# Kernel optimization log

Measured on AMD Instinct MI355X. Metric: run time of the kernel, lower is better.

## Reference

```python
import jax, jax.numpy as jnp
import numpy as np

B, S, HS = 2, 2048, 4096
NH, NKV = 32, 32
HD = HS // NH
INTER = 11008
VOCAB = 32000
EPS = 1e-6
ROPE_BASE = 10000.0


def setup_inputs() -> dict:
    key = jax.random.key(0)
    ks = jax.random.split(key, 16)
    sc = 0.02
    return {
        "hidden_states": jax.random.normal(ks[0], (B, S, HS), jnp.float32),
        "input_ids": jax.random.randint(ks[1], (B, S), 0, VOCAB, jnp.int32),
        "position_ids": jnp.arange(S, dtype=jnp.int32)[None, :],
        "embed": jax.random.normal(ks[2], (VOCAB, HS), jnp.float32) * sc,
        "fc_w": jax.random.normal(ks[3], (HS, 2 * HS), jnp.float32) * sc,
        "fc_b": jnp.zeros((HS,), jnp.float32),
        "q_w": jax.random.normal(ks[4], (NH * HD, HS), jnp.float32) * sc,
        "k_w": jax.random.normal(ks[5], (NKV * HD, HS), jnp.float32) * sc,
        "v_w": jax.random.normal(ks[6], (NKV * HD, HS), jnp.float32) * sc,
        "o_w": jax.random.normal(ks[7], (HS, NH * HD), jnp.float32) * sc,
        "gate_w": jax.random.normal(ks[8], (INTER, HS), jnp.float32) * sc,
        "up_w": jax.random.normal(ks[9], (INTER, HS), jnp.float32) * sc,
        "down_w": jax.random.normal(ks[10], (HS, INTER), jnp.float32) * sc,
        "post_ln_w": jnp.ones((HS,), jnp.float32),
    }


def _rotate_half(x):
    x1, x2 = jnp.split(x, 2, axis=-1)
    return jnp.concatenate((-x2, x1), axis=-1)


def _rms_norm(x, w, eps=EPS):
    x32 = x.astype(jnp.float32)
    x32 = x32 * jax.lax.rsqrt(jnp.mean(x32 * x32, axis=-1, keepdims=True) + eps)
    return (w * x32).astype(x.dtype)


def _forward(hidden_states, input_ids, position_ids, embed, fc_w, fc_b,
             q_w, k_w, v_w, o_w, gate_w, up_w, down_w, post_ln_w):
    # Embedding lookup (detached in original via no_grad)
    embeds = jax.lax.stop_gradient(embed[input_ids])  # [B,S,HS]
    h = jnp.concatenate((embeds, hidden_states), axis=-1) @ fc_w.T + fc_b  # [B,S,HS]

    # --- decoder layer 0 (no input_layernorm) ---
    residual = h
    q = (h @ q_w.T).reshape(B, S, NH, HD).transpose(0, 2, 1, 3)   # [B,NH,S,HD]
    k = (h @ k_w.T).reshape(B, S, NKV, HD).transpose(0, 2, 1, 3)
    v = (h @ v_w.T).reshape(B, S, NKV, HD).transpose(0, 2, 1, 3)

    # RoPE
    pos = position_ids[0].astype(jnp.float32)                      # [S]
    inv_freq = 1.0 / (ROPE_BASE ** (jnp.arange(0, HD, 2, dtype=jnp.float32) / HD))
    freqs = pos[:, None] * inv_freq[None, :]                       # [S,HD/2]
    emb = jnp.concatenate((freqs, freqs), axis=-1)                 # [S,HD]
    cos = jnp.cos(emb)[None, None, :, :]
    sin = jnp.sin(emb)[None, None, :, :]
    q = q * cos + _rotate_half(q) * sin
    k = k * cos + _rotate_half(k) * sin

    # attention (num_kv_groups == 1 here)
    scores = jnp.einsum('bhqd,bhkd->bhqk', q, k) / np.sqrt(HD)     # [B,NH,S,S]
    causal = jnp.triu(jnp.ones((S, S), bool), 1)
    scores = jnp.where(causal[None, None], -jnp.inf, scores)
    attn = jax.nn.softmax(scores.astype(jnp.float32), axis=-1).astype(q.dtype)
    out = jnp.einsum('bhqk,bhkd->bhqd', attn, v)                   # [B,NH,S,HD]
    out = out.transpose(0, 2, 1, 3).reshape(B, S, HS)
    attn_out = out @ o_w.T

    h = residual + attn_out
    residual = h
    hn = _rms_norm(h, post_ln_w)
    mlp = (jax.nn.silu(hn @ gate_w.T) * (hn @ up_w.T)) @ down_w.T
    return residual + mlp


def reference(hidden_states, input_ids, position_ids, embed, fc_w, fc_b,
              q_w, k_w, v_w, o_w, gate_w, up_w, down_w, post_ln_w):
    return _forward(hidden_states, input_ids, position_ids, embed, fc_w, fc_b,
                    q_w, k_w, v_w, o_w, gate_w, up_w, down_w, post_ln_w)
```

## Files before the change

kernel.cpp:

```cpp
#include <hip/hip_runtime.h>
#include <hip/hip_bf16.h>

typedef __attribute__((ext_vector_type(8))) short short8;
typedef __attribute__((ext_vector_type(4))) short short4v;
typedef __attribute__((ext_vector_type(4))) float floatx4;

#define B_SZ 2
#define S_SZ 2048
#define HS_SZ 4096
#define NH_SZ 32
#define HD_SZ 128
#define INTER_SZ 11008
#define M_TOT 4096

__device__ __forceinline__ float b2f(short s){
  unsigned int u = ((unsigned int)(unsigned short)s) << 16;
  return __builtin_bit_cast(float, u);
}
__device__ __forceinline__ short f2b(float f){
  unsigned int u = __builtin_bit_cast(unsigned int, f);
  u = (u + 0x7FFFu + ((u >> 16) & 1u)) >> 16;
  return (short)u;
}

typedef __attribute__((address_space(1))) const unsigned int gu32;
typedef __attribute__((address_space(3))) unsigned int lu32;
__device__ __forceinline__ void gl2lds16(const short* g, short* l){
  __builtin_amdgcn_global_load_lds((gu32*)g, (lu32*)l, 16, 0, 0);
}

#define BARRIER() asm volatile("s_barrier" ::: "memory")
#define WAITV8()  asm volatile("s_waitcnt vmcnt(8)" ::: "memory")
#define WAITV4()  asm volatile("s_waitcnt vmcnt(4)" ::: "memory")
#define WAITV2()  asm volatile("s_waitcnt vmcnt(2)" ::: "memory")
#define WAITV0()  asm volatile("s_waitcnt vmcnt(0)" ::: "memory")

__global__ void cvt_bf16_kernel(const float* __restrict__ src, short* __restrict__ dst, long n8){
  long idx = (long)blockIdx.x * blockDim.x + threadIdx.x;
  if (idx >= n8) return;
  long e = idx * 8;
  floatx4 v0 = *(const floatx4*)(src + e);
  floatx4 v1 = *(const floatx4*)(src + e + 4);
  short8 o;
  o[0]=f2b(v0[0]); o[1]=f2b(v0[1]); o[2]=f2b(v0[2]); o[3]=f2b(v0[3]);
  o[4]=f2b(v1[0]); o[5]=f2b(v1[1]); o[6]=f2b(v1[2]); o[7]=f2b(v1[3]);
  *(short8*)(dst + e) = o;
}

__global__ void embed_concat_kernel(const float* __restrict__ hidden,
                                    const int* __restrict__ ids,
                                    const float* __restrict__ embed,
                                    short* __restrict__ X0){
  long idx = (long)blockIdx.x * blockDim.x + threadIdx.x;
  const long total = (long)M_TOT * (2*HS_SZ) / 4;
  if (idx >= total) return;
  long e = idx * 4;
  int m = (int)(e / (2*HS_SZ));
  int c = (int)(e % (2*HS_SZ));
  const float* src;
  if (c < HS_SZ){
    src = embed + (long)ids[m]*HS_SZ + c;
  } else {
    src = hidden + (long)m*HS_SZ + (c - HS_SZ);
  }
  floatx4 v = *(const floatx4*)src;
  short4v o;
  o[0]=f2b(v[0]); o[1]=f2b(v[1]); o[2]=f2b(v[2]); o[3]=f2b(v[3]);
  *(short4v*)(X0 + e) = o;
}

#define G_STAGE(op,h,kof,qb) { \
  gl2lds16(gs[op][h] + (kof), lds + (qb) + (op)*16384 + (h)*8192 + wid*1024); \
  gl2lds16(gs[op][h] + k8 + (kof), lds + (qb) + (op)*16384 + (h)*8192 + wid*1024 + 512); }

#define LD_A(Mh,pb) { \
  _Pragma("unroll") \
  for (int mf=0; mf<4; mf++) \
    _Pragma("unroll") \
    for (int ks=0; ks<2; ks++) \
      af[mf][ks] = *(const short8*)(lds + (pb) + ((Mh)*128 + wr2*64 + mf*16 + lr)*64 + (((ks*4+lk)^lr7))*8); }

#define LD_B(BB,Nh,pb) { \
  _Pragma("unroll") \
  for (int nf=0; nf<2; nf++) \
    _Pragma("unroll") \
    for (int ks=0; ks<2; ks++) \
      BB[nf][ks] = *(const short8*)(lds + (pb) + 16384 + ((Nh)*128 + wc2*32 + nf*16 + lr)*64 + (((ks*4+lk)^lr7))*8); }

#define MMQ(Mh,Nh,BB) { \
  __builtin_amdgcn_s_setprio(1); \
  _Pragma("unroll") \
  for (int mf=0; mf<4; mf++) \
    _Pragma("unroll") \
    for (int nf=0; nf<2; nf++){ \
      acc[Mh][Nh][mf][nf] = __builtin_amdgcn_mfma_f32_16x16x32_bf16(af[mf][0], BB[nf][0], acc[Mh][Nh][mf][nf], 0,0,0); \
      acc[Mh][Nh][mf][nf] = __builtin_amdgcn_mfma_f32_16x16x32_bf16(af[mf][1], BB[nf][1], acc[Mh][Nh][mf][nf], 0,0,0); \
    } \
  __builtin_amdgcn_s_setprio(0); }

template<int EPI>
__global__ __launch_bounds__(512, 2)
void gemm256_kernel(const short* __restrict__ A, const short* __restrict__ Bw,
                    int M, int N, int K,
                    const float* __restrict__ bias,
                    const float* __restrict__ resid,
                    short* __restrict__ Cbf,
                    float* __restrict__ Cf){
  __shared__ __align__(16) short lds[65536];
  const int tid = threadIdx.x;
  const int wid = tid >> 6;
  const int lane = tid & 63;
  const int wr2 = wid >> 2, wc2 = wid & 3;
  const int lr = lane & 15, lk = lane >> 4;
  const int lr7 = lr & 7;

  const int nwg = gridDim.x * gridDim.y;
  const int id  = blockIdx.y * gridDim.x + blockIdx.x;
  const int cpx = nwg >> 3;
  const int sw  = (id & 7) * cpx + (id >> 3);
  const int bx  = sw % gridDim.x;
  const int by  = sw / gridDim.x;
  const int m0 = bx * 256, n0 = by * 256;

  const int srow = lane >> 3;
  const int sslot = (lane & 7) ^ srow;
  const long k8 = 8L * K;
  const short* gs[2][2];
  #pragma unroll
  for (int op=0; op<2; op++)
    #pragma unroll
    for (int h=0; h<2; h++){
      const int row = (op ? n0 : m0) + h*128 + wid*16 + srow;
      gs[op][h] = (op ? Bw : A) + (long)row*K + sslot*8;
    }

  floatx4 acc[2][2][4][2] = {};
  short8 af[4][2], b0[2][2], b1[2][2];
  const int nt = K >> 6;

  G_STAGE(0,0,0,0); G_STAGE(1,0,0,0); G_STAGE(1,1,0,0); G_STAGE(0,1,0,0);
  WAITV4(); BARRIER();

  for (int t = 0; t < nt-1; ++t){
    const int pb = (t & 1) << 15;
    const int qb = pb ^ 32768;
    const long kof = (long)(t+1) * 64;
    LD_A(0,pb); LD_B(b0,0,pb);
    G_STAGE(0,0,kof,qb);
    BARRIER();
    MMQ(0,0,b0);
    WAITV4(); BARRIER();
    LD_B(b1,1,pb);
    G_STAGE(1,0,kof,qb);
    BARRIER();
    MMQ(0,1,b1);
    WAITV4(); BARRIER();
    LD_A(1,pb);
    G_STAGE(1,1,kof,qb);
    BARRIER();
    MMQ(1,1,b1);
    BARRIER();
    G_STAGE(0,1,kof,qb);
    BARRIER();
    MMQ(1,0,b0);
    WAITV4(); BARRIER();
  }
  {
    const int pb = ((nt-1) & 1) << 15;
    LD_A(0,pb); LD_B(b0,0,pb);
    BARRIER(); MMQ(0,0,b0);
    WAITV2(); BARRIER();
    LD_B(b1,1,pb);
    BARRIER(); MMQ(0,1,b1);
    WAITV0(); BARRIER();
    LD_A(1,pb);
    BARRIER(); MMQ(1,1,b1);
    BARRIER();
    MMQ(1,0,b0);
  }

  #pragma unroll
  for (int Mh=0; Mh<2; Mh++){
    #pragma unroll
    for (int Nh=0; Nh<2; Nh++){
      #pragma unroll
      for (int mf=0; mf<4; mf++){
        #pragma unroll
        for (int nf=0; nf<2; nf++){
          const int col = n0 + Nh*128 + wc2*32 + nf*16 + lr;
          float bcol = (EPI==1) ? bias[col] : 0.0f;
          #pragma unroll
          for (int r=0; r<4; r++){
            const int row = m0 + Mh*128 + wr2*64 + mf*16 + lk*4 + r;
            float v = acc[Mh][Nh][mf][nf][r] + bcol;
            if (EPI==2) v += resid[(long)row*N + col];
            if (EPI==0 || EPI==1) Cbf[(long)row*N + col] = f2b(v);
            if (EPI==1 || EPI==2) Cf[(long)row*N + col] = v;
          }
        }
      }
    }
  }
}

__global__ void rope_kernel(short* __restrict__ q, short* __restrict__ k,
                            const int* __restrict__ pos_ids){
  long idx = (long)blockIdx.x * blockDim.x + threadIdx.x;
  const long total = (long)M_TOT * NH_SZ * (HD_SZ/2);
  if (idx >= total) return;
  int i  = (int)(idx & 63);
  long rh = idx >> 6;
  int h  = (int)(rh & 31);
  int m  = (int)(rh >> 5);
  int s  = m & (S_SZ - 1);
  float p = (float)pos_ids[s];
  const float L2_10000 = 13.28771237954945f;
  float inv = exp2f(-(2.0f*i/(float)HD_SZ) * L2_10000);
  float fr = p * inv;
  float sn, cs;
  sincosf(fr, &sn, &cs);
  long base = (long)m*HS_SZ + h*HD_SZ;
  short* qp = q + base;
  short* kp = k + base;
  float q1=b2f(qp[i]), q2=b2f(qp[i+64]);
  qp[i]    = f2b(q1*cs - q2*sn);
  qp[i+64] = f2b(q2*cs + q1*sn);
  float k1=b2f(kp[i]), k2=b2f(kp[i+64]);
  kp[i]    = f2b(k1*cs - k2*sn);
  kp[i+64] = f2b(k2*cs + k1*sn);
}

__global__ __launch_bounds__(256)
void vtrans_kernel(const short* __restrict__ V, short* __restrict__ VT){
  __shared__ short tile[64][68];
  const int s0 = blockIdx.x * 64;
  const int d0 = blockIdx.y * 64;
  const int bh = blockIdx.z;
  const int b = bh >> 5, h = bh & 31;
  const int tid = threadIdx.x;
  #pragma unroll
  for (int it=0; it<2; it++){
    int e = (it*256 + tid) * 8;
    int ss = e >> 6, col = e & 63;
    short8 v = *(const short8*)(V + ((long)(b*S_SZ + s0 + ss))*HS_SZ + h*HD_SZ + d0 + col);
    #pragma unroll
    for (int j=0;j<8;j++) tile[ss][col+j] = v[j];
  }
  __syncthreads();
  #pragma unroll
  for (int it=0; it<2; it++){
    int e = (it*256 + tid) * 8;
    int dd = e >> 6, scol = e & 63;
    short8 w;
    #pragma unroll
    for (int j=0;j<8;j++) w[j] = tile[scol+j][dd];
    *(short8*)(VT + ((long)(bh*HD_SZ + d0 + dd))*S_SZ + s0 + scol) = w;
  }
}

__global__ __launch_bounds__(256,2)
void attn_kernel(const short* __restrict__ Q, const short* __restrict__ K,
                 const short* __restrict__ VT, short* __restrict__ O){
  constexpr int LPD = 72;
  __shared__ __align__(16) short lds[32768];
  __shared__ __align__(16) short p_lds[4][16*LPD];
  const int bh = blockIdx.y;
  const int b = bh >> 5, h = bh & 31;
  const int q0 = blockIdx.x * 64;
  const int tid = threadIdx.x, wid = tid>>6, lane = tid&63;
  const int lr = lane & 15, lk = lane >> 4;
  const float scale = 0.08838834764831845f;

  const short* qbase = Q + ((long)(b*S_SZ + q0 + wid*16))*HS_SZ + h*HD_SZ;
  short8 qf[4];
  #pragma unroll
  for (int t=0;t<4;t++)
    qf[t] = *(const short8*)(qbase + (long)lr*HS_SZ + t*32 + lk*8);

  const short* kb[4]; const short* vb[4];
  int kloff[4], vloff[4];
  #pragma unroll
  for (int p=0;p<4;p++){
    const int seg = wid*4 + p;
    const int rowk = seg*4 + (lane >> 4);
    const int slotk = (lane & 15) ^ (rowk & 15);
    kb[p] = K + ((long)(b*S_SZ) + rowk)*HS_SZ + h*HD_SZ + slotk*8;
    kloff[p] = seg*512;
    const int dv = seg*8 + (lane >> 3);
    const int slotv = (lane & 7) ^ (dv & 7);
    vb[p] = VT + ((long)(bh*HD_SZ + dv))*S_SZ + slotv*8;
    vloff[p] = 8192 + seg*512;
  }

  floatx4 oacc[8] = {};
  float m_run[4] = {-1e30f,-1e30f,-1e30f,-1e30f};
  float l_run[4] = {0.f,0.f,0.f,0.f};

  const int nt = blockIdx.x + 1;

  #pragma unroll
  for (int p=0;p<4;p++){
    gl2lds16(kb[p], lds + kloff[p]);
    gl2lds16(vb[p], lds + vloff[p]);
  }

  for (int t=0; t<nt; ++t){
    const int dbase = (t & 1) * 16384;
    const int nbase = ((t+1) & 1) * 16384;
    if (t+1 < nt){
      const long kkn = (long)(t+1)*64*HS_SZ;
      const long vkn = (long)(t+1)*64;
      #pragma unroll
      for (int p=0;p<4;p++){
        gl2lds16(kb[p] + kkn, lds + nbase + kloff[p]);
        gl2lds16(vb[p] + vkn, lds + nbase + vloff[p]);
      }
      WAITV8();
    } else {
      WAITV0();
    }
    BARRIER();
    const int kv0 = t*64;
    floatx4 sfr[4];
    #pragma unroll
    for (int fn=0; fn<4; fn++){
      floatx4 s = {0.f,0.f,0.f,0.f};
      const int row = fn*16 + lr;
      #pragma unroll
      for (int tq=0; tq<4; tq++){
        short8 kf = *(const short8*)(lds + dbase + row*128 + (((tq*4+lk)^lr)&15)*8);
        s = __builtin_amdgcn_mfma_f32_16x16x32_bf16(qf[tq], kf, s, 0,0,0);
      }
      sfr[fn] = s;
    }
    float pv[4][4];
    #pragma unroll
    for (int fn=0; fn<4; fn++){
      const int col = kv0 + fn*16 + lr;
      #pragma unroll
      for (int r=0;r<4;r++){
        const int row = q0 + wid*16 + lk*4 + r;
        float sv = sfr[fn][r] * scale;
        pv[fn][r] = (col > row) ? -1e30f : sv;
      }
    }
    float mr4[4];
    int small = 1;
    #pragma unroll
    for (int r=0;r<4;r++){
      float mr = fmaxf(fmaxf(pv[0][r], pv[1][r]), fmaxf(pv[2][r], pv[3][r]));
      mr = fmaxf(mr, __shfl_xor(mr, 1, 16));
      mr = fmaxf(mr, __shfl_xor(mr, 2, 16));
      mr = fmaxf(mr, __shfl_xor(mr, 4, 16));
      mr = fmaxf(mr, __shfl_xor(mr, 8, 16));
      mr4[r] = mr;
      small &= (mr <= m_run[r] + 8.0f) ? 1 : 0;
    }
    const int skip = __all(small);
    float alpha_[4];
    #pragma unroll
    for (int r=0;r<4;r++){
      float mnew = skip ? m_run[r] : fmaxf(m_run[r], mr4[r]);
      alpha_[r] = skip ? 1.0f : __expf(m_run[r] - mnew);
      m_run[r] = mnew;
      float rs = 0.f;
      #pragma unroll
      for (int fn=0; fn<4; fn++){
        float e = __expf(pv[fn][r] - mnew);
        p_lds[wid][(lk*4+r)*LPD + fn*16 + lr] = f2b(e);
        rs += e;
      }
      rs += __shfl_xor(rs, 1, 16);
      rs += __shfl_xor(rs, 2, 16);
      rs += __shfl_xor(rs, 4, 16);
      rs += __shfl_xor(rs, 8, 16);
      l_run[r] = l_run[r]*alpha_[r] + rs;
    }
    if (!skip){
      #pragma unroll
      for (int f=0; f<8; f++){
        #pragma unroll
        for (int r=0;r<4;r++) oacc[f][r] *= alpha_[r];
      }
    }
    short8 pf[2];
    #pragma unroll
    for (int tp=0; tp<2; tp++)
      pf[tp] = *(const short8*)(&p_lds[wid][lr*LPD + tp*32 + lk*8]);
    #pragma unroll
    for (int f=0; f<8; f++){
      const int vrow = f*16 + lr;
      #pragma unroll
      for (int tp=0; tp<2; tp++){
        short8 vf = *(const short8*)(lds + dbase + 8192 + vrow*64 + (((tp*4+lk)^(lr&7))&7)*8);
        oacc[f] = __builtin_amdgcn_mfma_f32_16x16x32_bf16(pf[tp], vf, oacc[f], 0,0,0);
      }
    }
    BARRIER();
  }
  #pragma unroll
  for (int r=0;r<4;r++){
    const float inv = 1.0f / l_run[r];
    const long row = (long)(b*S_SZ + q0 + wid*16 + lk*4 + r);
    #pragma unroll
    for (int f=0; f<8; f++){
      O[row*HS_SZ + h*HD_SZ + f*16 + lr] = f2b(oacc[f][r]*inv);
    }
  }
}

__global__ void rmsnorm_kernel(const float* __restrict__ X, const float* __restrict__ W,
                               short* __restrict__ Y){
  const int row = blockIdx.x;
  const float* x = X + (long)row*HS_SZ;
  float ss = 0.f;
  for (int c = threadIdx.x*4; c < HS_SZ; c += 256*4){
    floatx4 v = *(const floatx4*)(x + c);
    ss += v[0]*v[0] + v[1]*v[1] + v[2]*v[2] + v[3]*v[3];
  }
  ss += __shfl_xor(ss, 32); ss += __shfl_xor(ss, 16);
  ss += __shfl_xor(ss, 8);  ss += __shfl_xor(ss, 4);
  ss += __shfl_xor(ss, 2);  ss += __shfl_xor(ss, 1);
  __shared__ float red[4];
  if ((threadIdx.x & 63) == 0) red[threadIdx.x >> 6] = ss;
  __syncthreads();
  ss = red[0] + red[1] + red[2] + red[3];
  const float rs = rsqrtf(ss / (float)HS_SZ + 1e-6f);
  for (int c = threadIdx.x*4; c < HS_SZ; c += 256*4){
    floatx4 v = *(const floatx4*)(x + c);
    floatx4 w = *(const floatx4*)(W + c);
    short4v o;
    o[0]=f2b(v[0]*rs*w[0]); o[1]=f2b(v[1]*rs*w[1]);
    o[2]=f2b(v[2]*rs*w[2]); o[3]=f2b(v[3]*rs*w[3]);
    *(short4v*)(Y + (long)row*HS_SZ + c) = o;
  }
}

__global__ void silu_mul_kernel(short* __restrict__ G, const short* __restrict__ U){
  long idx = (long)blockIdx.x * blockDim.x + threadIdx.x;
  const long total = (long)M_TOT * INTER_SZ / 8;
  if (idx >= total) return;
  long e = idx * 8;
  short8 g = *(short8*)(G + e);
  short8 u = *(const short8*)(U + e);
  short8 o;
  #pragma unroll
  for (int j=0;j<8;j++){
    float gf = b2f(g[j]);
    float uf = b2f(u[j]);
    float s = gf / (1.0f + __expf(-gf));
    o[j] = f2b(s * uf);
  }
  *(short8*)(G + e) = o;
}

extern "C" void kernel_launch(void* const* d_in, const int* in_sizes, int n_in,
                              void* d_out, int out_size, void* d_ws, size_t ws_size,
                              hipStream_t stream){
  (void)in_sizes; (void)n_in; (void)out_size;
  const float* hidden = (const float*)d_in[0];
  const int*   ids    = (const int*)d_in[1];
  const int*   pos    = (const int*)d_in[2];
  const float* embed  = (const float*)d_in[3];
  const float* fc_w   = (const float*)d_in[4];
  const float* fc_b   = (const float*)d_in[5];
  const float* q_w    = (const float*)d_in[6];
  const float* k_w    = (const float*)d_in[7];
  const float* v_w    = (const float*)d_in[8];
  const float* o_w    = (const float*)d_in[9];
  const float* gate_w = (const float*)d_in[10];
  const float* up_w   = (const float*)d_in[11];
  const float* down_w = (const float*)d_in[12];
  const float* ln_w   = (const float*)d_in[13];

  char* ws = (char*)d_ws;
  size_t off = 0;
  auto alloc = [&](size_t bytes)->char*{
    char* p = ws + off;
    off = (off + bytes + 255) & ~(size_t)255;
    return p;
  };
  short* wbf  = (short*)alloc((size_t)INTER_SZ*HS_SZ*2);
  short* X0   = (short*)alloc((size_t)M_TOT*2*HS_SZ*2);
  short* h_bf = (short*)alloc((size_t)M_TOT*HS_SZ*2);
  float* h_f  = (float*)alloc((size_t)M_TOT*HS_SZ*4);
  short* q_bf = (short*)alloc((size_t)M_TOT*HS_SZ*2);
  short* k_bf = (short*)alloc((size_t)M_TOT*HS_SZ*2);
  short* v_bf = (short*)alloc((size_t)M_TOT*HS_SZ*2);
  short* vt_bf= (short*)alloc((size_t)M_TOT*HS_SZ*2);
  short* a_bf = (short*)alloc((size_t)M_TOT*HS_SZ*2);
  float* h2_f = (float*)alloc((size_t)M_TOT*HS_SZ*4);
  short* hn_bf= (short*)alloc((size_t)M_TOT*HS_SZ*2);
  short* g_bf = (short*)alloc((size_t)M_TOT*INTER_SZ*2);
  short* u_bf = (short*)alloc((size_t)M_TOT*INTER_SZ*2);
  if (ws_size < off) return;

  auto cvt = [&](const float* src, short* dst, long n){
    long n8 = n / 8;
    cvt_bf16_kernel<<<(int)((n8 + 255)/256), 256, 0, stream>>>(src, dst, n8);
  };

  embed_concat_kernel<<<32768, 256, 0, stream>>>(hidden, ids, embed, X0);

  cvt(fc_w, wbf, (long)HS_SZ*2*HS_SZ);
  gemm256_kernel<1><<<dim3(16,16), 512, 0, stream>>>(X0, wbf, M_TOT, HS_SZ, 2*HS_SZ,
                                                     fc_b, nullptr, h_bf, h_f);
  cvt(q_w, wbf, (long)HS_SZ*HS_SZ);
  gemm256_kernel<0><<<dim3(16,16), 512, 0, stream>>>(h_bf, wbf, M_TOT, HS_SZ, HS_SZ,
                                                     nullptr, nullptr, q_bf, nullptr);
  cvt(k_w, wbf, (long)HS_SZ*HS_SZ);
  gemm256_kernel<0><<<dim3(16,16), 512, 0, stream>>>(h_bf, wbf, M_TOT, HS_SZ, HS_SZ,
                                                     nullptr, nullptr, k_bf, nullptr);
  cvt(v_w, wbf, (long)HS_SZ*HS_SZ);
  gemm256_kernel<0><<<dim3(16,16), 512, 0, stream>>>(h_bf, wbf, M_TOT, HS_SZ, HS_SZ,
                                                     nullptr, nullptr, v_bf, nullptr);
  rope_kernel<<<32768, 256, 0, stream>>>(q_bf, k_bf, pos);
  vtrans_kernel<<<dim3(S_SZ/64, HD_SZ/64, B_SZ*NH_SZ), 256, 0, stream>>>(v_bf, vt_bf);
  attn_kernel<<<dim3(S_SZ/64, B_SZ*NH_SZ), 256, 0, stream>>>(q_bf, k_bf, vt_bf, a_bf);
  cvt(o_w, wbf, (long)HS_SZ*HS_SZ);
  gemm256_kernel<2><<<dim3(16,16), 512, 0, stream>>>(a_bf, wbf, M_TOT, HS_SZ, HS_SZ,
                                                     nullptr, h_f, nullptr, h2_f);
  rmsnorm_kernel<<<M_TOT, 256, 0, stream>>>(h2_f, ln_w, hn_bf);
  cvt(gate_w, wbf, (long)INTER_SZ*HS_SZ);
  gemm256_kernel<0><<<dim3(16,43), 512, 0, stream>>>(hn_bf, wbf, M_TOT, INTER_SZ, HS_SZ,
                                                     nullptr, nullptr, g_bf, nullptr);
  cvt(up_w, wbf, (long)INTER_SZ*HS_SZ);
  gemm256_kernel<0><<<dim3(16,43), 512, 0, stream>>>(hn_bf, wbf, M_TOT, INTER_SZ, HS_SZ,
                                                     nullptr, nullptr, u_bf, nullptr);
  silu_mul_kernel<<<22016, 256, 0, stream>>>(g_bf, u_bf);
  cvt(down_w, wbf, (long)HS_SZ*INTER_SZ);
  gemm256_kernel<2><<<dim3(16,16), 512, 0, stream>>>(g_bf, wbf, M_TOT, HS_SZ, INTER_SZ,
                                                     nullptr, h2_f, nullptr, (float*)d_out);
}
```

Measured before the change: 2.279 ms.

## Fuse QKV projections and gate/up projections into single wide GEMMs

The three Q/K/V GEMMs become one GEMM with N=12288 over a concatenated weight buffer. The gate and up GEMMs become one GEMM with N=22016 that reads two weight pointers split at a row boundary. Downstream kernels (rope, vtrans, attention, silu_mul, down GEMM) now index the interleaved outputs through new leading-dimension parameters. This removes launch gaps and tail-wave underutilisation from several small grids and reuses activation tiles across a wider N, at the cost of strided output layouts and reusing workspace buffers (gu_bf, X0) to hold weights.

```diff
diff --git a/kernel.cpp b/kernel.cpp
--- a/kernel.cpp
+++ b/kernel.cpp
@@ -12,6 +12,8 @@
 #define HD_SZ 128
 #define INTER_SZ 11008
 #define M_TOT 4096
+#define QKV_N 12288
+#define GU_N 22016
 
 __device__ __forceinline__ float b2f(short s){
   unsigned int u = ((unsigned int)(unsigned short)s) << 16;
@@ -71,7 +73,7 @@
 
 #define G_STAGE(op,h,kof,qb) { \
   gl2lds16(gs[op][h] + (kof), lds + (qb) + (op)*16384 + (h)*8192 + wid*1024); \
-  gl2lds16(gs[op][h] + k8 + (kof), lds + (qb) + (op)*16384 + (h)*8192 + wid*1024 + 512); }
+  gl2lds16(gs[op][h] + k8o[op] + (kof), lds + (qb) + (op)*16384 + (h)*8192 + wid*1024 + 512); }
 
 #define LD_A(Mh,pb) { \
   _Pragma("unroll") \
@@ -101,7 +103,8 @@
 template<int EPI>
 __global__ __launch_bounds__(512, 2)
 void gemm256_kernel(const short* __restrict__ A, const short* __restrict__ Bw,
-                    int M, int N, int K,
+                    const short* __restrict__ Bw2, int nsplit,
+                    int K, int lda, int ldc,
                     const float* __restrict__ bias,
                     const float* __restrict__ resid,
                     short* __restrict__ Cbf,
@@ -124,15 +127,16 @@
 
   const int srow = lane >> 3;
   const int sslot = (lane & 7) ^ srow;
-  const long k8 = 8L * K;
+  const long k8o[2] = { 8L * lda, 8L * K };
   const short* gs[2][2];
   #pragma unroll
-  for (int op=0; op<2; op++)
-    #pragma unroll
-    for (int h=0; h<2; h++){
-      const int row = (op ? n0 : m0) + h*128 + wid*16 + srow;
-      gs[op][h] = (op ? Bw : A) + (long)row*K + sslot*8;
-    }
+  for (int h=0; h<2; h++){
+    const int rowa = m0 + h*128 + wid*16 + srow;
+    gs[0][h] = A + (long)rowa*lda + sslot*8;
+    const int rowb = n0 + h*128 + wid*16 + srow;
+    gs[1][h] = (rowb < nsplit ? Bw + (long)rowb*K
+                              : Bw2 + (long)(rowb - nsplit)*K) + sslot*8;
+  }
 
   floatx4 acc[2][2][4][2] = {};
   short8 af[4][2], b0[2][2], b1[2][2];
@@ -193,9 +197,9 @@
           for (int r=0; r<4; r++){
             const int row = m0 + Mh*128 + wr2*64 + mf*16 + lk*4 + r;
             float v = acc[Mh][Nh][mf][nf][r] + bcol;
-            if (EPI==2) v += resid[(long)row*N + col];
-            if (EPI==0 || EPI==1) Cbf[(long)row*N + col] = f2b(v);
-            if (EPI==1 || EPI==2) Cf[(long)row*N + col] = v;
+            if (EPI==2) v += resid[(long)row*ldc + col];
+            if (EPI==0 || EPI==1) Cbf[(long)row*ldc + col] = f2b(v);
+            if (EPI==1 || EPI==2) Cf[(long)row*ldc + col] = v;
           }
         }
       }
@@ -203,8 +207,7 @@
   }
 }
 
-__global__ void rope_kernel(short* __restrict__ q, short* __restrict__ k,
-                            const int* __restrict__ pos_ids){
+__global__ void rope_kernel(short* __restrict__ qkv, const int* __restrict__ pos_ids){
   long idx = (long)blockIdx.x * blockDim.x + threadIdx.x;
   const long total = (long)M_TOT * NH_SZ * (HD_SZ/2);
   if (idx >= total) return;
@@ -219,9 +222,8 @@
   float fr = p * inv;
   float sn, cs;
   sincosf(fr, &sn, &cs);
-  long base = (long)m*HS_SZ + h*HD_SZ;
-  short* qp = q + base;
-  short* kp = k + base;
+  short* qp = qkv + (long)m*QKV_N + h*HD_SZ;
+  short* kp = qp + HS_SZ;
   float q1=b2f(qp[i]), q2=b2f(qp[i+64]);
   qp[i]    = f2b(q1*cs - q2*sn);
   qp[i+64] = f2b(q2*cs + q1*sn);
@@ -231,7 +233,7 @@
 }
 
 __global__ __launch_bounds__(256)
-void vtrans_kernel(const short* __restrict__ V, short* __restrict__ VT){
+void vtrans_kernel(const short* __restrict__ QKV, short* __restrict__ VT){
   __shared__ short tile[64][68];
   const int s0 = blockIdx.x * 64;
   const int d0 = blockIdx.y * 64;
@@ -242,7 +244,7 @@
   for (int it=0; it<2; it++){
     int e = (it*256 + tid) * 8;
     int ss = e >> 6, col = e & 63;
-    short8 v = *(const short8*)(V + ((long)(b*S_SZ + s0 + ss))*HS_SZ + h*HD_SZ + d0 + col);
+    short8 v = *(const short8*)(QKV + ((long)(b*S_SZ + s0 + ss))*QKV_N + 2*HS_SZ + h*HD_SZ + d0 + col);
     #pragma unroll
     for (int j=0;j<8;j++) tile[ss][col+j] = v[j];
   }
@@ -259,8 +261,8 @@
 }
 
 __global__ __launch_bounds__(256,2)
-void attn_kernel(const short* __restrict__ Q, const short* __restrict__ K,
-                 const short* __restrict__ VT, short* __restrict__ O){
+void attn_kernel(const short* __restrict__ QKV, const short* __restrict__ VT,
+                 short* __restrict__ O){
   constexpr int LPD = 72;
   __shared__ __align__(16) short lds[32768];
   __shared__ __align__(16) short p_lds[4][16*LPD];
@@ -271,11 +273,11 @@
   const int lr = lane & 15, lk = lane >> 4;
   const float scale = 0.08838834764831845f;
 
-  const short* qbase = Q + ((long)(b*S_SZ + q0 + wid*16))*HS_SZ + h*HD_SZ;
+  const short* qbase = QKV + ((long)(b*S_SZ + q0 + wid*16))*QKV_N + h*HD_SZ;
   short8 qf[4];
   #pragma unroll
   for (int t=0;t<4;t++)
-    qf[t] = *(const short8*)(qbase + (long)lr*HS_SZ + t*32 + lk*8);
+    qf[t] = *(const short8*)(qbase + (long)lr*QKV_N + t*32 + lk*8);
 
   const short* kb[4]; const short* vb[4];
   int kloff[4], vloff[4];
@@ -284,7 +286,7 @@
     const int seg = wid*4 + p;
     const int rowk = seg*4 + (lane >> 4);
     const int slotk = (lane & 15) ^ (rowk & 15);
-    kb[p] = K + ((long)(b*S_SZ) + rowk)*HS_SZ + h*HD_SZ + slotk*8;
+    kb[p] = QKV + ((long)(b*S_SZ) + rowk)*QKV_N + HS_SZ + h*HD_SZ + slotk*8;
     kloff[p] = seg*512;
     const int dv = seg*8 + (lane >> 3);
     const int slotv = (lane & 7) ^ (dv & 7);
@@ -308,7 +310,7 @@
     const int dbase = (t & 1) * 16384;
     const int nbase = ((t+1) & 1) * 16384;
     if (t+1 < nt){
-      const long kkn = (long)(t+1)*64*HS_SZ;
+      const long kkn = (long)(t+1)*64*QKV_N;
       const long vkn = (long)(t+1)*64;
       #pragma unroll
       for (int p=0;p<4;p++){
@@ -436,13 +438,16 @@
   }
 }
 
-__global__ void silu_mul_kernel(short* __restrict__ G, const short* __restrict__ U){
+__global__ void silu_mul_kernel(short* __restrict__ GU){
   long idx = (long)blockIdx.x * blockDim.x + threadIdx.x;
   const long total = (long)M_TOT * INTER_SZ / 8;
   if (idx >= total) return;
   long e = idx * 8;
-  short8 g = *(short8*)(G + e);
-  short8 u = *(const short8*)(U + e);
+  int m = (int)(e / INTER_SZ);
+  int i = (int)(e - (long)m*INTER_SZ);
+  long gix = (long)m*GU_N + i;
+  short8 g = *(short8*)(GU + gix);
+  short8 u = *(const short8*)(GU + gix + INTER_SZ);
   short8 o;
   #pragma unroll
   for (int j=0;j<8;j++){
@@ -451,7 +456,7 @@
     float s = gf / (1.0f + __expf(-gf));
     o[j] = f2b(s * uf);
   }
-  *(short8*)(G + e) = o;
+  *(short8*)(GU + gix) = o;
 }
 
 extern "C" void kernel_launch(void* const* d_in, const int* in_sizes, int n_in,
@@ -480,20 +485,20 @@
     off = (off + bytes + 255) & ~(size_t)255;
     return p;
   };
-  short* wbf  = (short*)alloc((size_t)INTER_SZ*HS_SZ*2);
-  short* X0   = (short*)alloc((size_t)M_TOT*2*HS_SZ*2);
-  short* h_bf = (short*)alloc((size_t)M_TOT*HS_SZ*2);
-  float* h_f  = (float*)alloc((size_t)M_TOT*HS_SZ*4);
-  short* q_bf = (short*)alloc((size_t)M_TOT*HS_SZ*2);
-  short* k_bf = (short*)alloc((size_t)M_TOT*HS_SZ*2);
-  short* v_bf = (short*)alloc((size_t)M_TOT*HS_SZ*2);
-  short* vt_bf= (short*)alloc((size_t)M_TOT*HS_SZ*2);
-  short* a_bf = (short*)alloc((size_t)M_TOT*HS_SZ*2);
-  float* h2_f = (float*)alloc((size_t)M_TOT*HS_SZ*4);
-  short* hn_bf= (short*)alloc((size_t)M_TOT*HS_SZ*2);
-  short* g_bf = (short*)alloc((size_t)M_TOT*INTER_SZ*2);
-  short* u_bf = (short*)alloc((size_t)M_TOT*INTER_SZ*2);
+  short* wbf   = (short*)alloc((size_t)INTER_SZ*HS_SZ*2);
+  short* X0    = (short*)alloc((size_t)M_TOT*2*HS_SZ*2);
+  short* h_bf  = (short*)alloc((size_t)M_TOT*HS_SZ*2);
+  float* h_f   = (float*)alloc((size_t)M_TOT*HS_SZ*4);
+  short* qkv_bf= (short*)alloc((size_t)M_TOT*QKV_N*2);
+  short* vt_bf = (short*)alloc((size_t)M_TOT*HS_SZ*2);
+  short* a_bf  = (short*)alloc((size_t)M_TOT*HS_SZ*2);
+  float* h2_f  = (float*)alloc((size_t)M_TOT*HS_SZ*4);
+  short* hn_bf = (short*)alloc((size_t)M_TOT*HS_SZ*2);
+  short* gu_bf = (short*)alloc((size_t)M_TOT*GU_N*2);
   if (ws_size < off) return;
+
+  short* wqkv   = gu_bf;
+  short* wgate  = X0;
 
   auto cvt = [&](const float* src, short* dst, long n){
     long n8 = n / 8;
@@ -503,32 +508,31 @@
   embed_concat_kernel<<<32768, 256, 0, stream>>>(hidden, ids, embed, X0);
 
   cvt(fc_w, wbf, (long)HS_SZ*2*HS_SZ);
-  gemm256_kernel<1><<<dim3(16,16), 512, 0, stream>>>(X0, wbf, M_TOT, HS_SZ, 2*HS_SZ,
+  gemm256_kernel<1><<<dim3(16,16), 512, 0, stream>>>(X0, wbf, nullptr, 1<<30,
+                                                     2*HS_SZ, 2*HS_SZ, HS_SZ,
                                                      fc_b, nullptr, h_bf, h_f);
-  cvt(q_w, wbf, (long)HS_SZ*HS_SZ);
-  gemm256_kernel<0><<<dim3(16,16), 512, 0, stream>>>(h_bf, wbf, M_TOT, HS_SZ, HS_SZ,
-                                                     nullptr, nullptr, q_bf, nullptr);
-  cvt(k_w, wbf, (long)HS_SZ*HS_SZ);
-  gemm256_kernel<0><<<dim3(16,16), 512, 0, stream>>>(h_bf, wbf, M_TOT, HS_SZ, HS_SZ,
-                                                     nullptr, nullptr, k_bf, nullptr);
-  cvt(v_w, wbf, (long)HS_SZ*HS_SZ);
-  gemm256_kernel<0><<<dim3(16,16), 512, 0, stream>>>(h_bf, wbf, M_TOT, HS_SZ, HS_SZ,
-                                                     nullptr, nullptr, v_bf, nullptr);
-  rope_kernel<<<32768, 256, 0, stream>>>(q_bf, k_bf, pos);
-  vtrans_kernel<<<dim3(S_SZ/64, HD_SZ/64, B_SZ*NH_SZ), 256, 0, stream>>>(v_bf, vt_bf);
-  attn_kernel<<<dim3(S_SZ/64, B_SZ*NH_SZ), 256, 0, stream>>>(q_bf, k_bf, vt_bf, a_bf);
+  cvt(q_w, wqkv,                       (long)HS_SZ*HS_SZ);
+  cvt(k_w, wqkv + (long)HS_SZ*HS_SZ,   (long)HS_SZ*HS_SZ);
+  cvt(v_w, wqkv + 2L*HS_SZ*HS_SZ,      (long)HS_SZ*HS_SZ);
+  gemm256_kernel<0><<<dim3(16,48), 512, 0, stream>>>(h_bf, wqkv, nullptr, 1<<30,
+                                                     HS_SZ, HS_SZ, QKV_N,
+                                                     nullptr, nullptr, qkv_bf, nullptr);
+  rope_kernel<<<32768, 256, 0, stream>>>(qkv_bf, pos);
+  vtrans_kernel<<<dim3(S_SZ/64, HD_SZ/64, B_SZ*NH_SZ), 256, 0, stream>>>(qkv_bf, vt_bf);
+  attn_kernel<<<dim3(S_SZ/64, B_SZ*NH_SZ), 256, 0, stream>>>(qkv_bf, vt_bf, a_bf);
   cvt(o_w, wbf, (long)HS_SZ*HS_SZ);
-  gemm256_kernel<2><<<dim3(16,16), 512, 0, stream>>>(a_bf, wbf, M_TOT, HS_SZ, HS_SZ,
+  gemm256_kernel<2><<<dim3(16,16), 512, 0, stream>>>(a_bf, wbf, nullptr, 1<<30,
+                                                     HS_SZ, HS_SZ, HS_SZ,
                                                      nullptr, h_f, nullptr, h2_f);
   rmsnorm_kernel<<<M_TOT, 256, 0, stream>>>(h2_f, ln_w, hn_bf);
-  cvt(gate_w, wbf, (long)INTER_SZ*HS_SZ);
-  gemm256_kernel<0><<<dim3(16,43), 512, 0, stream>>>(hn_bf, wbf, M_TOT, INTER_SZ, HS_SZ,
-                                                     nullptr, nullptr, g_bf, nullptr);
-  cvt(up_w, wbf, (long)INTER_SZ*HS_SZ);
-  gemm256_kernel<0><<<dim3(16,43), 512, 0, stream>>>(hn_bf, wbf, M_TOT, INTER_SZ, HS_SZ,
-                                                     nullptr, nullptr, u_bf, nullptr);
-  silu_mul_kernel<<<22016, 256, 0, stream>>>(g_bf, u_bf);
+  cvt(gate_w, wgate, (long)INTER_SZ*HS_SZ);
+  cvt(up_w,   wbf,   (long)INTER_SZ*HS_SZ);
+  gemm256_kernel<0><<<dim3(16,86), 512, 0, stream>>>(hn_bf, wgate, wbf, INTER_SZ,
+                                                     HS_SZ, HS_SZ, GU_N,
+                                                     nullptr, nullptr, gu_bf, nullptr);
+  silu_mul_kernel<<<22016, 256, 0, stream>>>(gu_bf);
   cvt(down_w, wbf, (long)HS_SZ*INTER_SZ);
-  gemm256_kernel<2><<<dim3(16,16), 512, 0, stream>>>(g_bf, wbf, M_TOT, HS_SZ, INTER_SZ,
+  gemm256_kernel<2><<<dim3(16,16), 512, 0, stream>>>(gu_bf, wbf, nullptr, 1<<30,
+                                                     INTER_SZ, GU_N, HS_SZ,
                                                      nullptr, h2_f, nullptr, (float*)d_out);
 }
```

After: 2.294 ms. Within noise of the previous version (+0.7%).
